# Performance work log

Hardware: AMD Instinct MI355X
Metric: run time of the kernel (lower is better)

Reference implementation:

```python
import jax, jax.numpy as jnp
import numpy as np
import math

B, H, S, D = 1, 8, 2048, 64
LAMBDA_INIT = 0.8 - 0.6 * math.exp(-0.3)  # depth=1
EPS = 1e-5


def _clin(xr, xi, wr, wi, br, bi):
    # complex linear: (wr + i*wi)(xr + i*xi)
    out_r = xr @ wr.T - xi @ wi.T + br
    out_i = xr @ wi.T + xi @ wr.T + bi
    return out_r, out_i


def setup_inputs() -> dict:
    ks = jax.random.split(jax.random.key(0), 24)
    n = lambda i, shp, s=1.0: jax.random.normal(ks[i], shp, jnp.float32) * s
    inv = 1.0 / math.sqrt(D)
    return {
        'q_r': n(0, (B, H, S, D)), 'q_i': n(1, (B, H, S, D)),
        'k_r': n(2, (B, H, S, D)), 'k_i': n(3, (B, H, S, D)),
        'v_r': n(4, (B, H, S, D)), 'v_i': n(5, (B, H, S, D)),
        'pe_q_r': n(6, (B, H, S, D)), 'pe_q_i': n(7, (B, H, S, D)),
        'pe_k_r': n(8, (B, H, S, D)), 'pe_k_i': n(9, (B, H, S, D)),
        'qwr': n(10, (2 * D, D), inv), 'qwi': n(11, (2 * D, D), inv),
        'qbr': jnp.zeros(2 * D), 'qbi': jnp.zeros(2 * D),
        'kwr': n(12, (D, D), inv), 'kwi': n(13, (D, D), inv),
        'kbr': jnp.zeros(D), 'kbi': jnp.zeros(D),
        'vwr': n(14, (D, D), inv), 'vwi': n(15, (D, D), inv),
        'vbr': jnp.zeros(D), 'vbi': jnp.zeros(D),
        'gwr': n(16, (D, D), inv), 'gwi': n(17, (D, D), inv),
        'gbr': jnp.zeros(D), 'gbi': jnp.zeros(D),
        'owr': n(18, (D, D), inv), 'owi': n(19, (D, D), inv),
        'obr': jnp.zeros(D), 'obi': jnp.zeros(D),
        'lq1': n(20, (H,), 0.1), 'lk1': n(21, (H,), 0.1),
        'lq2': n(22, (H,), 0.1), 'lk2': n(23, (H,), 0.1),
        'subw': jnp.ones(2 * D),
    }


def _forward(q_r, q_i, k_r, k_i, v_r, v_i, pe_q_r, pe_q_i, pe_k_r, pe_k_i,
             qwr, qwi, qbr, qbi, kwr, kwi, kbr, kbi, vwr, vwi, vbr, vbi,
             gwr, gwi, gbr, gbi, owr, owi, obr, obi,
             lq1, lk1, lq2, lk2, subw):
    b, h, s, d = q_r.shape
    scale = d ** (-0.5)
    qpr, qpi = _clin(q_r, q_i, qwr, qwi, qbr, qbi)      # [b,h,s,2d]
    kpr, kpi = _clin(k_r, k_i, kwr, kwi, kbr, kbi)      # [b,h,s,d]
    vpr, vpi = _clin(v_r, v_i, vwr, vwi, vbr, vbi)      # [b,h,s,d]
    qpr = qpr + jnp.concatenate([pe_q_r, pe_q_r], -1)
    qpi = qpi + jnp.concatenate([pe_q_i, pe_q_i], -1)
    kpr = kpr + pe_k_r
    kpi = kpi + pe_k_i
    # split two physical heads: view(..., d, 2) interleaves last dim
    qpr = qpr.reshape(b, h, s, d, 2)
    qpi = qpi.reshape(b, h, s, d, 2)
    q1r, q2r = qpr[..., 0], qpr[..., 1]
    q1i, q2i = qpi[..., 0], qpi[..., 1]

    def attn(qr, qi):
        sr = jnp.einsum('bhqd,bhkd->bhqk', qr, kpr) + jnp.einsum('bhqd,bhkd->bhqk', qi, kpi)
        si = jnp.einsum('bhqd,bhkd->bhqk', qi, kpr) - jnp.einsum('bhqd,bhkd->bhqk', qr, kpi)
        scores = jnp.sqrt(sr * sr + si * si + 1e-8) * scale
        return jax.nn.softmax(scores, axis=-1)

    a1 = attn(q1r, q1i)
    a2 = attn(q2r, q2i)
    o1r = a1 @ vpr; o1i = a1 @ vpi
    o2r = a2 @ vpr; o2i = a2 @ vpi
    # NOTE: torch computes a lambda-weighted difference here but immediately
    # overwrites it with the normed slice below, so it never reaches the output.
    cr = jnp.stack([o1r, o2r], -1).reshape(b, h, s, 2 * d)
    ci = jnp.stack([o1i, o2i], -1).reshape(b, h, s, 2 * d)
    rms = jnp.sqrt(jnp.mean(cr * cr + ci * ci, axis=-1, keepdims=True) + EPS)
    nr = cr / rms * subw
    ni = ci / rms * subw
    ar = nr[..., :d]
    ai = ni[..., :d]
    gr, gi = _clin(q_r, q_i, gwr, gwi, gbr, gbi)
    xr = gr * ar - gi * ai
    xi = gr * ai + gi * ar
    out_r, out_i = _clin(xr, xi, owr, owi, obr, obi)
    return out_r, out_i, gr, gi


def reference(q_r, q_i, k_r, k_i, v_r, v_i, pe_q_r, pe_q_i, pe_k_r, pe_k_i,
              qwr, qwi, qbr, qbi, kwr, kwi, kbr, kbi, vwr, vwi, vbr, vbi,
              gwr, gwi, gbr, gbi, owr, owi, obr, obi,
              lq1, lk1, lq2, lk2, subw):
    return _forward(q_r, q_i, k_r, k_i, v_r, v_i, pe_q_r, pe_q_i, pe_k_r, pe_k_i,
                    qwr, qwi, qbr, qbi, kwr, kwi, kbr, kbi, vwr, vwi, vbr, vbi,
                    gwr, gwi, gbr, gbi, owr, owi, obr, obi,
                    lq1, lk1, lq2, lk2, subw)
```

## Files before the change

kernel.cpp:

```cpp
#include <hip/hip_runtime.h>
#include <hip/hip_bf16.h>

#define NH 8
#define SQ 2048
#define HD 64
#define NTOT (NH * SQ * HD)
#define PIT 72

typedef unsigned short u16;
typedef unsigned int u32;
typedef __attribute__((ext_vector_type(8))) unsigned short us8;
typedef __attribute__((ext_vector_type(4))) unsigned short us4v;
typedef __attribute__((ext_vector_type(8))) _Float16 h8;
typedef __attribute__((ext_vector_type(4))) float f4;
typedef __attribute__((ext_vector_type(4))) u32 u4;

#define MFMA_F16 __builtin_amdgcn_mfma_f32_16x16x32_f16

__device__ __forceinline__ u16 f2h(float f) {
    union { _Float16 h; u16 u; } c; c.h = (_Float16)f; return c.u;
}
__device__ __forceinline__ float h2f(u16 u) {
    union { _Float16 h; u16 u; } c; c.u = u; return (float)c.h;
}
__device__ __forceinline__ h8 neg_h8(h8 a) {
    union { h8 h; u4 u; } c; c.h = a;
    c.u ^= 0x80008000u;
    return c.h;
}
__device__ __forceinline__ h8 pack8h(const float* p) {
    float4 a = ((const float4*)p)[0];
    float4 b = ((const float4*)p)[1];
    h8 r;
    r[0] = (_Float16)a.x; r[1] = (_Float16)a.y; r[2] = (_Float16)a.z; r[3] = (_Float16)a.w;
    r[4] = (_Float16)b.x; r[5] = (_Float16)b.y; r[6] = (_Float16)b.z; r[7] = (_Float16)b.w;
    return r;
}

__device__ __forceinline__ int swz8(int row, int chunk) {
    return row * 64 + ((chunk ^ (row & 7)) << 3);
}

struct Afrag { h8 r0, r1, i0, i1, ni0, ni1; };

__global__ __launch_bounds__(256) void proj_kernel(
    const float* __restrict__ q_r, const float* __restrict__ q_i,
    const float* __restrict__ k_r, const float* __restrict__ k_i,
    const float* __restrict__ v_r, const float* __restrict__ v_i,
    const float* __restrict__ pe_q_r, const float* __restrict__ pe_q_i,
    const float* __restrict__ pe_k_r, const float* __restrict__ pe_k_i,
    const float* __restrict__ qwr, const float* __restrict__ qwi,
    const float* __restrict__ qbr, const float* __restrict__ qbi,
    const float* __restrict__ kwr, const float* __restrict__ kwi,
    const float* __restrict__ kbr, const float* __restrict__ kbi,
    const float* __restrict__ vwr, const float* __restrict__ vwi,
    const float* __restrict__ vbr, const float* __restrict__ vbi,
    const float* __restrict__ gwr, const float* __restrict__ gwi,
    const float* __restrict__ gbr, const float* __restrict__ gbi,
    u16* __restrict__ q1r, u16* __restrict__ q1i,
    u16* __restrict__ q2r, u16* __restrict__ q2i,
    u16* __restrict__ kpr, u16* __restrict__ kpi,
    u16* __restrict__ vtr, u16* __restrict__ vti,
    float* __restrict__ out_gr, float* __restrict__ out_gi)
{
    const int t = threadIdx.x;
    const int wv = t >> 6, l = t & 63;
    const int quad = l >> 4, m16 = l & 15;
    const int rowbase = blockIdx.x * 16;
    const int arow = rowbase + m16;
    const int h = rowbase >> 11;
    const int c0 = quad * 8;

    auto loadA = [&](const float* pr, const float* pi) {
        Afrag a;
        const float* rp = pr + arow * 64;
        const float* ip = pi + arow * 64;
        a.r0 = pack8h(rp + c0);      a.r1 = pack8h(rp + 32 + c0);
        a.i0 = pack8h(ip + c0);      a.i1 = pack8h(ip + 32 + c0);
        a.ni0 = neg_h8(a.i0);        a.ni1 = neg_h8(a.i1);
        return a;
    };

    auto ctile = [&](const Afrag& A, const float* wr, const float* wi, int cb,
                     f4& Cr, f4& Ci) {
        const float* wrp = wr + (cb + m16) * 64;
        const float* wip = wi + (cb + m16) * 64;
        h8 Br0 = pack8h(wrp + c0), Br1 = pack8h(wrp + 32 + c0);
        h8 Bi0 = pack8h(wip + c0), Bi1 = pack8h(wip + 32 + c0);
        Cr = (f4)0.f; Ci = (f4)0.f;
        Cr = MFMA_F16(A.r0,  Br0, Cr, 0, 0, 0);
        Cr = MFMA_F16(A.r1,  Br1, Cr, 0, 0, 0);
        Cr = MFMA_F16(A.ni0, Bi0, Cr, 0, 0, 0);
        Cr = MFMA_F16(A.ni1, Bi1, Cr, 0, 0, 0);
        Ci = MFMA_F16(A.r0,  Bi0, Ci, 0, 0, 0);
        Ci = MFMA_F16(A.r1,  Bi1, Ci, 0, 0, 0);
        Ci = MFMA_F16(A.i0,  Br0, Ci, 0, 0, 0);
        Ci = MFMA_F16(A.i1,  Br1, Ci, 0, 0, 0);
    };

    auto qtile = [&](const Afrag& A, int nt) {
        f4 Cr, Ci;
        ctile(A, qwr, qwi, nt * 16, Cr, Ci);
        int c = nt * 16 + m16;
        float br = qbr[c], bi = qbi[c];
        int dd = c >> 1, pc = c & 63;
        u16* dR = (c & 1) ? q2r : q1r;
        u16* dI = (c & 1) ? q2i : q1i;
        #pragma unroll
        for (int r = 0; r < 4; ++r) {
            int g = rowbase + quad * 4 + r;
            dR[g * 64 + dd] = f2h(Cr[r] + br + pe_q_r[g * 64 + pc]);
            dI[g * 64 + dd] = f2h(Ci[r] + bi + pe_q_i[g * 64 + pc]);
        }
    };
    auto ktile = [&](const Afrag& A, int nt) {
        f4 Cr, Ci;
        ctile(A, kwr, kwi, nt * 16, Cr, Ci);
        int c = nt * 16 + m16;
        float br = kbr[c], bi = kbi[c];
        #pragma unroll
        for (int r = 0; r < 4; ++r) {
            int g = rowbase + quad * 4 + r;
            kpr[g * 64 + c] = f2h(Cr[r] + br + pe_k_r[g * 64 + c]);
            kpi[g * 64 + c] = f2h(Ci[r] + bi + pe_k_i[g * 64 + c]);
        }
    };
    auto vtile = [&](const Afrag& A, int nt) {
        f4 Cr, Ci;
        ctile(A, vwr, vwi, nt * 16, Cr, Ci);
        int c = nt * 16 + m16;
        float br = vbr[c], bi = vbi[c];
        int s0 = (rowbase & 2047) + quad * 4;
        size_t tix = (size_t)(h * 64 + c) * 2048 + s0;
        us4v pr, pi;
        #pragma unroll
        for (int r = 0; r < 4; ++r) {
            pr[r] = f2h(Cr[r] + br);
            pi[r] = f2h(Ci[r] + bi);
        }
        *(us4v*)&vtr[tix] = pr;
        *(us4v*)&vti[tix] = pi;
    };
    auto gtile = [&](const Afrag& A, int nt) {
        f4 Cr, Ci;
        ctile(A, gwr, gwi, nt * 16, Cr, Ci);
        int c = nt * 16 + m16;
        float br = gbr[c], bi = gbi[c];
        #pragma unroll
        for (int r = 0; r < 4; ++r) {
            int g = rowbase + quad * 4 + r;
            out_gr[g * 64 + c] = Cr[r] + br;
            out_gi[g * 64 + c] = Ci[r] + bi;
        }
    };

    if (wv == 0) {
        Afrag Aq = loadA(q_r, q_i);
        qtile(Aq, 0); qtile(Aq, 1); qtile(Aq, 2); qtile(Aq, 3); qtile(Aq, 4);
    } else if (wv == 1) {
        Afrag Aq = loadA(q_r, q_i);
        qtile(Aq, 5); qtile(Aq, 6); qtile(Aq, 7);
        gtile(Aq, 0); gtile(Aq, 1);
    } else if (wv == 2) {
        Afrag Ak = loadA(k_r, k_i);
        ktile(Ak, 0); ktile(Ak, 1); ktile(Ak, 2); ktile(Ak, 3);
        Afrag Aq = loadA(q_r, q_i);
        gtile(Aq, 2);
    } else {
        Afrag Av = loadA(v_r, v_i);
        vtile(Av, 0); vtile(Av, 1); vtile(Av, 2); vtile(Av, 3);
        Afrag Aq = loadA(q_r, q_i);
        gtile(Aq, 3);
    }
}

__global__ __launch_bounds__(256) void attn_kernel(
    const u16* __restrict__ q1r, const u16* __restrict__ q1i,
    const u16* __restrict__ q2r, const u16* __restrict__ q2i,
    const u16* __restrict__ kpr, const u16* __restrict__ kpi,
    const u16* __restrict__ vtr, const u16* __restrict__ vti,
    u16* __restrict__ o1r, u16* __restrict__ o1i,
    u16* __restrict__ o2r, u16* __restrict__ o2i)
{
    __shared__ __align__(16) u16 Kr[64 * 64], Ki[64 * 64];
    __shared__ __align__(16) u16 Vr[64 * 64], Vi[64 * 64];
    __shared__ __align__(16) u16 Pb[64 * 64];

    const int t  = threadIdx.x;
    const int qt = blockIdx.x;
    const int br = blockIdx.y;
    const int h  = blockIdx.z;

    const int wq   = t >> 6;
    const int l    = t & 63;
    const int quad = l >> 4;
    const int m    = l & 15;

    const u16* Qsr = br ? q2r : q1r;
    const u16* Qsi = br ? q2i : q1i;
    const int hbase = h * SQ * 64;
    const int qbase = hbase + qt * 64 * 64;
    const int vbase = h * 64 * SQ;

    const u16* qrr = Qsr + qbase + (wq * 16 + m) * 64;
    const u16* qri = Qsi + qbase + (wq * 16 + m) * 64;
    h8 Qr0 = *(const h8*)(qrr + quad * 8);
    h8 Qr1 = *(const h8*)(qrr + 32 + quad * 8);
    h8 Qi0 = *(const h8*)(qri + quad * 8);
    h8 Qi1 = *(const h8*)(qri + 32 + quad * 8);
    h8 nQr0 = neg_h8(Qr0);
    h8 nQr1 = neg_h8(Qr1);

    const int sr0 = t >> 3;
    const int sc  = t & 7;
    us8 rK0, rK1, rC0, rC1, rV0, rV1, rW0, rW1;

    auto issue = [&](int kt) {
        const int kb = hbase + kt * 4096;
        const int vb = vbase + kt * 64;
        const int sc8 = sc * 8;
        rK0 = *(const us8*)(kpr + kb + sr0 * 64 + sc8);
        rK1 = *(const us8*)(kpr + kb + (sr0 + 32) * 64 + sc8);
        rC0 = *(const us8*)(kpi + kb + sr0 * 64 + sc8);
        rC1 = *(const us8*)(kpi + kb + (sr0 + 32) * 64 + sc8);
        rV0 = *(const us8*)(vtr + vb + sr0 * SQ + sc8);
        rV1 = *(const us8*)(vtr + vb + (sr0 + 32) * SQ + sc8);
        rW0 = *(const us8*)(vti + vb + sr0 * SQ + sc8);
        rW1 = *(const us8*)(vti + vb + (sr0 + 32) * SQ + sc8);
    };
    auto commit = [&]() {
        const int o0 = swz8(sr0, sc);
        const int o1 = swz8(sr0 + 32, sc);
        *(us8*)&Kr[o0] = rK0;  *(us8*)&Kr[o1] = rK1;
        *(us8*)&Ki[o0] = rC0;  *(us8*)&Ki[o1] = rC1;
        *(us8*)&Vr[o0] = rV0;  *(us8*)&Vr[o1] = rV1;
        *(us8*)&Vi[o0] = rW0;  *(us8*)&Vi[o1] = rW1;
    };

    float mreg[4], Lp[4];
    #pragma unroll
    for (int r = 0; r < 4; ++r) { mreg[r] = -1e30f; Lp[r] = 0.f; }
    f4 Ovr[4], Ovi[4];
    #pragma unroll
    for (int d = 0; d < 4; ++d) { Ovr[d] = (f4)0.f; Ovi[d] = (f4)0.f; }

    issue(0);

    for (int kt = 0; kt < 32; ++kt) {
        __syncthreads();
        commit();
        if (kt < 31) issue(kt + 1);
        __syncthreads();

        float sv[4][4];
        #pragma unroll
        for (int nt = 0; nt < 4; ++nt) {
            const int kr = nt * 16 + m;
            h8 k0 = *(const h8*)&Kr[swz8(kr, quad)];
            h8 k1 = *(const h8*)&Kr[swz8(kr, quad + 4)];
            h8 c0 = *(const h8*)&Ki[swz8(kr, quad)];
            h8 c1 = *(const h8*)&Ki[swz8(kr, quad + 4)];
            f4 ar = (f4)0.f, ai = (f4)0.f;
            __builtin_amdgcn_s_setprio(1);
            ar = MFMA_F16(Qr0, k0, ar, 0, 0, 0);
            ar = MFMA_F16(Qr1, k1, ar, 0, 0, 0);
            ar = MFMA_F16(Qi0, c0, ar, 0, 0, 0);
            ar = MFMA_F16(Qi1, c1, ar, 0, 0, 0);
            ai = MFMA_F16(Qi0, k0, ai, 0, 0, 0);
            ai = MFMA_F16(Qi1, k1, ai, 0, 0, 0);
            ai = MFMA_F16(nQr0, c0, ai, 0, 0, 0);
            ai = MFMA_F16(nQr1, c1, ai, 0, 0, 0);
            __builtin_amdgcn_s_setprio(0);
            #pragma unroll
            for (int r = 0; r < 4; ++r)
                sv[nt][r] = __builtin_amdgcn_sqrtf(ar[r] * ar[r] + ai[r] * ai[r] + 1e-8f) * 0.125f;
        }

        float rv[4];
        #pragma unroll
        for (int r = 0; r < 4; ++r) {
            float x = fmaxf(fmaxf(sv[0][r], sv[1][r]), fmaxf(sv[2][r], sv[3][r]));
            x = fmaxf(x, __shfl_xor(x, 1));
            x = fmaxf(x, __shfl_xor(x, 2));
            x = fmaxf(x, __shfl_xor(x, 4));
            x = fmaxf(x, __shfl_xor(x, 8));
            rv[r] = x;
        }

        bool need = (rv[0] > mreg[0] + 8.f) | (rv[1] > mreg[1] + 8.f) |
                    (rv[2] > mreg[2] + 8.f) | (rv[3] > mreg[3] + 8.f);
        if (__any(need)) {
            #pragma unroll
            for (int r = 0; r < 4; ++r) {
                float mn = fmaxf(mreg[r], rv[r]);
                float al = __expf(mreg[r] - mn);
                mreg[r] = mn;
                Lp[r] *= al;
                #pragma unroll
                for (int dtr = 0; dtr < 4; ++dtr) { Ovr[dtr][r] *= al; Ovi[dtr][r] *= al; }
            }
        }

        #pragma unroll
        for (int r = 0; r < 4; ++r) {
            const int prow = wq * 16 + quad * 4 + r;
            #pragma unroll
            for (int nt = 0; nt < 4; ++nt) {
                float p = __expf(sv[nt][r] - mreg[r]);
                Lp[r] += p;
                const int col = nt * 16 + m;
                Pb[swz8(prow, col >> 3) + (col & 7)] = f2h(p);
            }
        }

        const int qrow = wq * 16 + m;
        h8 pa0 = *(const h8*)&Pb[swz8(qrow, quad)];
        h8 pa1 = *(const h8*)&Pb[swz8(qrow, quad + 4)];

        #pragma unroll
        for (int dt = 0; dt < 4; ++dt) {
            const int vr_ = dt * 16 + m;
            h8 b0 = *(const h8*)&Vr[swz8(vr_, quad)];
            h8 b1 = *(const h8*)&Vr[swz8(vr_, quad + 4)];
            h8 d0 = *(const h8*)&Vi[swz8(vr_, quad)];
            h8 d1 = *(const h8*)&Vi[swz8(vr_, quad + 4)];
            __builtin_amdgcn_s_setprio(1);
            Ovr[dt] = MFMA_F16(pa0, b0, Ovr[dt], 0, 0, 0);
            Ovr[dt] = MFMA_F16(pa1, b1, Ovr[dt], 0, 0, 0);
            Ovi[dt] = MFMA_F16(pa0, d0, Ovi[dt], 0, 0, 0);
            Ovi[dt] = MFMA_F16(pa1, d1, Ovi[dt], 0, 0, 0);
            __builtin_amdgcn_s_setprio(0);
        }
    }

    {
        #pragma unroll
        for (int r = 0; r < 4; ++r) {
            float x = Lp[r];
            x += __shfl_xor(x, 1);
            x += __shfl_xor(x, 2);
            x += __shfl_xor(x, 4);
            x += __shfl_xor(x, 8);
            Lp[r] = x;
        }
        u16* Dr = br ? o2r : o1r;
        u16* Di = br ? o2i : o1i;
        float inv[4];
        #pragma unroll
        for (int r = 0; r < 4; ++r) inv[r] = 1.f / Lp[r];
        #pragma unroll
        for (int dt = 0; dt < 4; ++dt) {
            #pragma unroll
            for (int r = 0; r < 4; ++r) {
                int q = wq * 16 + quad * 4 + r;
                Dr[qbase + q * 64 + dt * 16 + m] = f2h(Ovr[dt][r] * inv[r]);
                Di[qbase + q * 64 + dt * 16 + m] = f2h(Ovi[dt][r] * inv[r]);
            }
        }
    }
}

__global__ __launch_bounds__(256) void epi_kernel(
    const u16* __restrict__ o1r, const u16* __restrict__ o1i,
    const u16* __restrict__ o2r, const u16* __restrict__ o2i,
    const float* __restrict__ out_gr, const float* __restrict__ out_gi,
    const float* __restrict__ subw,
    const float* __restrict__ owr, const float* __restrict__ owi,
    const float* __restrict__ obr, const float* __restrict__ obi,
    float* __restrict__ out_r, float* __restrict__ out_i)
{
    __shared__ __align__(16) u16 L1r[16][64], L1i[16][64];
    __shared__ __align__(16) u16 L2r[16][64], L2i[16][64];
    __shared__ __align__(16) u16 Xr[16][PIT], Xi[16][PIT];

    const int t = threadIdx.x;
    const int rowbase = blockIdx.x * 16;

    {
        int r = t >> 4, c4 = (t & 15) * 4;
        size_t gi = (size_t)(rowbase + r) * 64 + c4;
        *(us4v*)&L1r[r][c4] = *(const us4v*)(o1r + gi);
        *(us4v*)&L1i[r][c4] = *(const us4v*)(o1i + gi);
        *(us4v*)&L2r[r][c4] = *(const us4v*)(o2r + gi);
        *(us4v*)&L2i[r][c4] = *(const us4v*)(o2i + gi);
    }
    __syncthreads();

    {
        int r = t >> 4, c4 = (t & 15) * 4;
        float ss = 0.f;
        #pragma unroll
        for (int j = 0; j < 4; ++j) {
            float a = h2f(L1r[r][c4 + j]), b = h2f(L1i[r][c4 + j]);
            float c = h2f(L2r[r][c4 + j]), d = h2f(L2i[r][c4 + j]);
            ss += a * a + b * b + c * c + d * d;
        }
        ss += __shfl_xor(ss, 1);
        ss += __shfl_xor(ss, 2);
        ss += __shfl_xor(ss, 4);
        ss += __shfl_xor(ss, 8);
        float inv = 1.f / sqrtf(ss * (1.f / 128.f) + 1e-5f);

        float4 g_r = *(const float4*)(out_gr + (size_t)(rowbase + r) * 64 + c4);
        float4 g_i = *(const float4*)(out_gi + (size_t)(rowbase + r) * 64 + c4);
        const float* grv = (const float*)&g_r;
        const float* giv = (const float*)&g_i;

        us4v xrp, xip;
        #pragma unroll
        for (int j = 0; j < 4; ++j) {
            int c = c4 + j;
            int s = c >> 1;
            float cr_ = (c & 1) ? h2f(L2r[r][s]) : h2f(L1r[r][s]);
            float ci_ = (c & 1) ? h2f(L2i[r][s]) : h2f(L1i[r][s]);
            float sw = subw[c];
            float ar_ = cr_ * inv * sw;
            float ai_ = ci_ * inv * sw;
            xrp[j] = f2h(grv[j] * ar_ - giv[j] * ai_);
            xip[j] = f2h(grv[j] * ai_ + giv[j] * ar_);
        }
        *(us4v*)&Xr[r][c4] = xrp;
        *(us4v*)&Xi[r][c4] = xip;
    }
    __syncthreads();

    const int wv = t >> 6, l = t & 63;
    const int quad = l >> 4, m16 = l & 15;
    const int c0 = quad * 8;

    h8 Ar0 = *(const h8*)&Xr[m16][c0];
    h8 Ar1 = *(const h8*)&Xr[m16][32 + c0];
    h8 Ai0 = *(const h8*)&Xi[m16][c0];
    h8 Ai1 = *(const h8*)&Xi[m16][32 + c0];
    h8 nAi0 = neg_h8(Ai0), nAi1 = neg_h8(Ai1);

    const int c = wv * 16 + m16;
    const float* wrp = owr + c * 64;
    const float* wip = owi + c * 64;
    h8 Br0 = pack8h(wrp + c0), Br1 = pack8h(wrp + 32 + c0);
    h8 Bi0 = pack8h(wip + c0), Bi1 = pack8h(wip + 32 + c0);

    f4 Cr = (f4)0.f, Ci = (f4)0.f;
    Cr = MFMA_F16(Ar0,  Br0, Cr, 0, 0, 0);
    Cr = MFMA_F16(Ar1,  Br1, Cr, 0, 0, 0);
    Cr = MFMA_F16(nAi0, Bi0, Cr, 0, 0, 0);
    Cr = MFMA_F16(nAi1, Bi1, Cr, 0, 0, 0);
    Ci = MFMA_F16(Ar0,  Bi0, Ci, 0, 0, 0);
    Ci = MFMA_F16(Ar1,  Bi1, Ci, 0, 0, 0);
    Ci = MFMA_F16(Ai0,  Br0, Ci, 0, 0, 0);
    Ci = MFMA_F16(Ai1,  Br1, Ci, 0, 0, 0);

    float br_ = obr[c], bi_ = obi[c];
    #pragma unroll
    for (int r = 0; r < 4; ++r) {
        size_t g = (size_t)(rowbase + quad * 4 + r) * 64 + c;
        out_r[g] = Cr[r] + br_;
        out_i[g] = Ci[r] + bi_;
    }
}

extern "C" void kernel_launch(void* const* d_in, const int* in_sizes, int n_in,
                              void* d_out, int out_size, void* d_ws, size_t ws_size,
                              hipStream_t stream)
{
    (void)in_sizes; (void)n_in; (void)out_size; (void)ws_size;

    float* out    = (float*)d_out;
    float* out_r  = out;
    float* out_i  = out + (size_t)NTOT;
    float* out_gr = out + 2 * (size_t)NTOT;
    float* out_gi = out + 3 * (size_t)NTOT;

    char* w = (char*)d_ws;
    const size_t N = (size_t)NTOT;
    u16* q1r = (u16*)w; w += N * 2;
    u16* q1i = (u16*)w; w += N * 2;
    u16* q2r = (u16*)w; w += N * 2;
    u16* q2i = (u16*)w; w += N * 2;
    u16* kpr = (u16*)w; w += N * 2;
    u16* kpi = (u16*)w; w += N * 2;
    u16* vtr = (u16*)w; w += N * 2;
    u16* vti = (u16*)w; w += N * 2;
    u16* o1r = (u16*)w; w += N * 2;
    u16* o1i = (u16*)w; w += N * 2;
    u16* o2r = (u16*)w; w += N * 2;
    u16* o2i = (u16*)w; w += N * 2;

    proj_kernel<<<dim3(1024), dim3(256), 0, stream>>>(
        (const float*)d_in[0], (const float*)d_in[1],
        (const float*)d_in[2], (const float*)d_in[3],
        (const float*)d_in[4], (const float*)d_in[5],
        (const float*)d_in[6], (const float*)d_in[7],
        (const float*)d_in[8], (const float*)d_in[9],
        (const float*)d_in[10], (const float*)d_in[11],
        (const float*)d_in[12], (const float*)d_in[13],
        (const float*)d_in[14], (const float*)d_in[15],
        (const float*)d_in[16], (const float*)d_in[17],
        (const float*)d_in[18], (const float*)d_in[19],
        (const float*)d_in[20], (const float*)d_in[21],
        (const float*)d_in[22], (const float*)d_in[23],
        (const float*)d_in[24], (const float*)d_in[25],
        q1r, q1i, q2r, q2i, kpr, kpi, vtr, vti, out_gr, out_gi);

    attn_kernel<<<dim3(SQ / 64, 2, NH), dim3(256), 0, stream>>>(
        q1r, q1i, q2r, q2i, kpr, kpi, vtr, vti, o1r, o1i, o2r, o2i);

    epi_kernel<<<dim3(1024), dim3(256), 0, stream>>>(
        o1r, o1i, o2r, o2i, out_gr, out_gi,
        (const float*)d_in[34], (const float*)d_in[26], (const float*)d_in[27],
        (const float*)d_in[28], (const float*)d_in[29],
        out_r, out_i);
}
```

Before: 264.1 us.

## Load K/V fragments directly from global memory instead of LDS staging

New measurement: 406.9 us. +54.1%, slower.

```diff
diff --git a/kernel.cpp b/kernel.cpp
--- a/kernel.cpp
+++ b/kernel.cpp
@@ -182,8 +182,6 @@
     u16* __restrict__ o1r, u16* __restrict__ o1i,
     u16* __restrict__ o2r, u16* __restrict__ o2i)
 {
-    __shared__ __align__(16) u16 Kr[64 * 64], Ki[64 * 64];
-    __shared__ __align__(16) u16 Vr[64 * 64], Vi[64 * 64];
     __shared__ __align__(16) u16 Pb[64 * 64];
 
     const int t  = threadIdx.x;
@@ -211,31 +209,10 @@
     h8 nQr0 = neg_h8(Qr0);
     h8 nQr1 = neg_h8(Qr1);
 
-    const int sr0 = t >> 3;
-    const int sc  = t & 7;
-    us8 rK0, rK1, rC0, rC1, rV0, rV1, rW0, rW1;
-
-    auto issue = [&](int kt) {
-        const int kb = hbase + kt * 4096;
-        const int vb = vbase + kt * 64;
-        const int sc8 = sc * 8;
-        rK0 = *(const us8*)(kpr + kb + sr0 * 64 + sc8);
-        rK1 = *(const us8*)(kpr + kb + (sr0 + 32) * 64 + sc8);
-        rC0 = *(const us8*)(kpi + kb + sr0 * 64 + sc8);
-        rC1 = *(const us8*)(kpi + kb + (sr0 + 32) * 64 + sc8);
-        rV0 = *(const us8*)(vtr + vb + sr0 * SQ + sc8);
-        rV1 = *(const us8*)(vtr + vb + (sr0 + 32) * SQ + sc8);
-        rW0 = *(const us8*)(vti + vb + sr0 * SQ + sc8);
-        rW1 = *(const us8*)(vti + vb + (sr0 + 32) * SQ + sc8);
-    };
-    auto commit = [&]() {
-        const int o0 = swz8(sr0, sc);
-        const int o1 = swz8(sr0 + 32, sc);
-        *(us8*)&Kr[o0] = rK0;  *(us8*)&Kr[o1] = rK1;
-        *(us8*)&Ki[o0] = rC0;  *(us8*)&Ki[o1] = rC1;
-        *(us8*)&Vr[o0] = rV0;  *(us8*)&Vr[o1] = rV1;
-        *(us8*)&Vi[o0] = rW0;  *(us8*)&Vi[o1] = rW1;
-    };
+    const u16* bKr = kpr + hbase + m * 64 + quad * 8;
+    const u16* bKi = kpi + hbase + m * 64 + quad * 8;
+    const u16* bVr = vtr + vbase + m * 2048 + quad * 8;
+    const u16* bVi = vti + vbase + m * 2048 + quad * 8;
 
     float mreg[4], Lp[4];
     #pragma unroll
@@ -244,22 +221,14 @@
     #pragma unroll
     for (int d = 0; d < 4; ++d) { Ovr[d] = (f4)0.f; Ovi[d] = (f4)0.f; }
 
-    issue(0);
-
     for (int kt = 0; kt < 32; ++kt) {
-        __syncthreads();
-        commit();
-        if (kt < 31) issue(kt + 1);
-        __syncthreads();
-
         float sv[4][4];
         #pragma unroll
         for (int nt = 0; nt < 4; ++nt) {
-            const int kr = nt * 16 + m;
-            h8 k0 = *(const h8*)&Kr[swz8(kr, quad)];
-            h8 k1 = *(const h8*)&Kr[swz8(kr, quad + 4)];
-            h8 c0 = *(const h8*)&Ki[swz8(kr, quad)];
-            h8 c1 = *(const h8*)&Ki[swz8(kr, quad + 4)];
+            h8 k0 = *(const h8*)(bKr + nt * 1024);
+            h8 k1 = *(const h8*)(bKr + nt * 1024 + 32);
+            h8 c0 = *(const h8*)(bKi + nt * 1024);
+            h8 c1 = *(const h8*)(bKi + nt * 1024 + 32);
             f4 ar = (f4)0.f, ai = (f4)0.f;
             __builtin_amdgcn_s_setprio(1);
             ar = MFMA_F16(Qr0, k0, ar, 0, 0, 0);
@@ -275,6 +244,7 @@
             for (int r = 0; r < 4; ++r)
                 sv[nt][r] = __builtin_amdgcn_sqrtf(ar[r] * ar[r] + ai[r] * ai[r] + 1e-8f) * 0.125f;
         }
+        bKr += 4096; bKi += 4096;
 
         float rv[4];
         #pragma unroll
@@ -319,11 +289,10 @@
 
         #pragma unroll
         for (int dt = 0; dt < 4; ++dt) {
-            const int vr_ = dt * 16 + m;
-            h8 b0 = *(const h8*)&Vr[swz8(vr_, quad)];
-            h8 b1 = *(const h8*)&Vr[swz8(vr_, quad + 4)];
-            h8 d0 = *(const h8*)&Vi[swz8(vr_, quad)];
-            h8 d1 = *(const h8*)&Vi[swz8(vr_, quad + 4)];
+            h8 b0 = *(const h8*)(bVr + dt * 32768);
+            h8 b1 = *(const h8*)(bVr + dt * 32768 + 32);
+            h8 d0 = *(const h8*)(bVi + dt * 32768);
+            h8 d1 = *(const h8*)(bVi + dt * 32768 + 32);
             __builtin_amdgcn_s_setprio(1);
             Ovr[dt] = MFMA_F16(pa0, b0, Ovr[dt], 0, 0, 0);
             Ovr[dt] = MFMA_F16(pa1, b1, Ovr[dt], 0, 0, 0);
@@ -331,6 +300,7 @@
             Ovi[dt] = MFMA_F16(pa1, d1, Ovi[dt], 0, 0, 0);
             __builtin_amdgcn_s_setprio(0);
         }
+        bVr += 64; bVi += 64;
     }
 
     {
```

## Process both head branches per block to share K/V tiles

Applied to the files above, without the earlier changes.

After: 294.1 us. 11.4% more time.

```diff
diff --git a/kernel.cpp b/kernel.cpp
--- a/kernel.cpp
+++ b/kernel.cpp
@@ -174,7 +174,7 @@
     }
 }
 
-__global__ __launch_bounds__(256) void attn_kernel(
+__global__ __launch_bounds__(256, 1) void attn_kernel(
     const u16* __restrict__ q1r, const u16* __restrict__ q1i,
     const u16* __restrict__ q2r, const u16* __restrict__ q2i,
     const u16* __restrict__ kpr, const u16* __restrict__ kpi,
@@ -184,14 +184,15 @@
 {
     __shared__ __align__(16) u16 Kr[64 * 64], Ki[64 * 64];
     __shared__ __align__(16) u16 Vr[64 * 64], Vi[64 * 64];
-    __shared__ __align__(16) u16 Pb[64 * 64];
+    __shared__ __align__(16) u16 Pb[128 * 64];
 
     const int t  = threadIdx.x;
     const int qt = blockIdx.x;
-    const int br = blockIdx.y;
     const int h  = blockIdx.z;
 
     const int wq   = t >> 6;
+    const int br   = wq >> 1;
+    const int rh   = wq & 1;
     const int l    = t & 63;
     const int quad = l >> 4;
     const int m    = l & 15;
@@ -202,14 +203,18 @@
     const int qbase = hbase + qt * 64 * 64;
     const int vbase = h * 64 * SQ;
 
-    const u16* qrr = Qsr + qbase + (wq * 16 + m) * 64;
-    const u16* qri = Qsi + qbase + (wq * 16 + m) * 64;
-    h8 Qr0 = *(const h8*)(qrr + quad * 8);
-    h8 Qr1 = *(const h8*)(qrr + 32 + quad * 8);
-    h8 Qi0 = *(const h8*)(qri + quad * 8);
-    h8 Qi1 = *(const h8*)(qri + 32 + quad * 8);
-    h8 nQr0 = neg_h8(Qr0);
-    h8 nQr1 = neg_h8(Qr1);
+    h8 Qr0[2], Qr1[2], Qi0[2], Qi1[2], nQr0[2], nQr1[2];
+    #pragma unroll
+    for (int rs = 0; rs < 2; ++rs) {
+        const u16* qrr = Qsr + qbase + (rh * 32 + rs * 16 + m) * 64;
+        const u16* qri = Qsi + qbase + (rh * 32 + rs * 16 + m) * 64;
+        Qr0[rs] = *(const h8*)(qrr + quad * 8);
+        Qr1[rs] = *(const h8*)(qrr + 32 + quad * 8);
+        Qi0[rs] = *(const h8*)(qri + quad * 8);
+        Qi1[rs] = *(const h8*)(qri + 32 + quad * 8);
+        nQr0[rs] = neg_h8(Qr0[rs]);
+        nQr1[rs] = neg_h8(Qr1[rs]);
+    }
 
     const int sr0 = t >> 3;
     const int sc  = t & 7;
@@ -237,12 +242,16 @@
         *(us8*)&Vi[o0] = rW0;  *(us8*)&Vi[o1] = rW1;
     };
 
-    float mreg[4], Lp[4];
+    float mreg[2][4], Lp[2][4];
     #pragma unroll
-    for (int r = 0; r < 4; ++r) { mreg[r] = -1e30f; Lp[r] = 0.f; }
-    f4 Ovr[4], Ovi[4];
+    for (int rs = 0; rs < 2; ++rs)
+        #pragma unroll
+        for (int r = 0; r < 4; ++r) { mreg[rs][r] = -1e30f; Lp[rs][r] = 0.f; }
+    f4 Ovr[2][4], Ovi[2][4];
     #pragma unroll
-    for (int d = 0; d < 4; ++d) { Ovr[d] = (f4)0.f; Ovi[d] = (f4)0.f; }
+    for (int rs = 0; rs < 2; ++rs)
+        #pragma unroll
+        for (int d = 0; d < 4; ++d) { Ovr[rs][d] = (f4)0.f; Ovi[rs][d] = (f4)0.f; }
 
     issue(0);
 
@@ -252,7 +261,7 @@
         if (kt < 31) issue(kt + 1);
         __syncthreads();
 
-        float sv[4][4];
+        float sv[2][4][4];
         #pragma unroll
         for (int nt = 0; nt < 4; ++nt) {
             const int kr = nt * 16 + m;
@@ -260,62 +269,78 @@
             h8 k1 = *(const h8*)&Kr[swz8(kr, quad + 4)];
             h8 c0 = *(const h8*)&Ki[swz8(kr, quad)];
             h8 c1 = *(const h8*)&Ki[swz8(kr, quad + 4)];
-            f4 ar = (f4)0.f, ai = (f4)0.f;
             __builtin_amdgcn_s_setprio(1);
-            ar = MFMA_F16(Qr0, k0, ar, 0, 0, 0);
-            ar = MFMA_F16(Qr1, k1, ar, 0, 0, 0);
-            ar = MFMA_F16(Qi0, c0, ar, 0, 0, 0);
-            ar = MFMA_F16(Qi1, c1, ar, 0, 0, 0);
-            ai = MFMA_F16(Qi0, k0, ai, 0, 0, 0);
-            ai = MFMA_F16(Qi1, k1, ai, 0, 0, 0);
-            ai = MFMA_F16(nQr0, c0, ai, 0, 0, 0);
-            ai = MFMA_F16(nQr1, c1, ai, 0, 0, 0);
+            #pragma unroll
+            for (int rs = 0; rs < 2; ++rs) {
+                f4 ar = (f4)0.f, ai = (f4)0.f;
+                ar = MFMA_F16(Qr0[rs], k0, ar, 0, 0, 0);
+                ar = MFMA_F16(Qr1[rs], k1, ar, 0, 0, 0);
+                ar = MFMA_F16(Qi0[rs], c0, ar, 0, 0, 0);
+                ar = MFMA_F16(Qi1[rs], c1, ar, 0, 0, 0);
+                ai = MFMA_F16(Qi0[rs], k0, ai, 0, 0, 0);
+                ai = MFMA_F16(Qi1[rs], k1, ai, 0, 0, 0);
+                ai = MFMA_F16(nQr0[rs], c0, ai, 0, 0, 0);
+                ai = MFMA_F16(nQr1[rs], c1, ai, 0, 0, 0);
+                #pragma unroll
+                for (int r = 0; r < 4; ++r)
+                    sv[rs][nt][r] =
+                        __builtin_amdgcn_sqrtf(ar[r] * ar[r] + ai[r] * ai[r] + 1e-8f) * 0.125f;
+            }
             __builtin_amdgcn_s_setprio(0);
-            #pragma unroll
-            for (int r = 0; r < 4; ++r)
-                sv[nt][r] = __builtin_amdgcn_sqrtf(ar[r] * ar[r] + ai[r] * ai[r] + 1e-8f) * 0.125f;
-        }
-
-        float rv[4];
-        #pragma unroll
-        for (int r = 0; r < 4; ++r) {
-            float x = fmaxf(fmaxf(sv[0][r], sv[1][r]), fmaxf(sv[2][r], sv[3][r]));
-            x = fmaxf(x, __shfl_xor(x, 1));
-            x = fmaxf(x, __shfl_xor(x, 2));
-            x = fmaxf(x, __shfl_xor(x, 4));
-            x = fmaxf(x, __shfl_xor(x, 8));
-            rv[r] = x;
-        }
-
-        bool need = (rv[0] > mreg[0] + 8.f) | (rv[1] > mreg[1] + 8.f) |
-                    (rv[2] > mreg[2] + 8.f) | (rv[3] > mreg[3] + 8.f);
+        }
+
+        float rv[2][4];
+        bool need = false;
+        #pragma unroll
+        for (int rs = 0; rs < 2; ++rs)
+            #pragma unroll
+            for (int r = 0; r < 4; ++r) {
+                float x = fmaxf(fmaxf(sv[rs][0][r], sv[rs][1][r]),
+                                fmaxf(sv[rs][2][r], sv[rs][3][r]));
+                x = fmaxf(x, __shfl_xor(x, 1));
+                x = fmaxf(x, __shfl_xor(x, 2));
+                x = fmaxf(x, __shfl_xor(x, 4));
+                x = fmaxf(x, __shfl_xor(x, 8));
+                rv[rs][r] = x;
+                need |= (x > mreg[rs][r] + 8.f);
+            }
         if (__any(need)) {
             #pragma unroll
+            for (int rs = 0; rs < 2; ++rs)
+                #pragma unroll
+                for (int r = 0; r < 4; ++r) {
+                    float mn = fmaxf(mreg[rs][r], rv[rs][r]);
+                    float al = __expf(mreg[rs][r] - mn);
+                    mreg[rs][r] = mn;
+                    Lp[rs][r] *= al;
+                    #pragma unroll
+                    for (int dt = 0; dt < 4; ++dt) {
+                        Ovr[rs][dt][r] *= al; Ovi[rs][dt][r] *= al;
+                    }
+                }
+        }
+
+        #pragma unroll
+        for (int rs = 0; rs < 2; ++rs)
+            #pragma unroll
             for (int r = 0; r < 4; ++r) {
-                float mn = fmaxf(mreg[r], rv[r]);
-                float al = __expf(mreg[r] - mn);
-                mreg[r] = mn;
-                Lp[r] *= al;
+                const int prow = wq * 32 + rs * 16 + quad * 4 + r;
                 #pragma unroll
-                for (int dtr = 0; dtr < 4; ++dtr) { Ovr[dtr][r] *= al; Ovi[dtr][r] *= al; }
+                for (int nt = 0; nt < 4; ++nt) {
+                    float p = __expf(sv[rs][nt][r] - mreg[rs][r]);
+                    Lp[rs][r] += p;
+                    const int col = nt * 16 + m;
+                    Pb[swz8(prow, col >> 3) + (col & 7)] = f2h(p);
+                }
             }
-        }
-
-        #pragma unroll
-        for (int r = 0; r < 4; ++r) {
-            const int prow = wq * 16 + quad * 4 + r;
-            #pragma unroll
-            for (int nt = 0; nt < 4; ++nt) {
-                float p = __expf(sv[nt][r] - mreg[r]);
-                Lp[r] += p;
-                const int col = nt * 16 + m;
-                Pb[swz8(prow, col >> 3) + (col & 7)] = f2h(p);
-            }
-        }
-
-        const int qrow = wq * 16 + m;
-        h8 pa0 = *(const h8*)&Pb[swz8(qrow, quad)];
-        h8 pa1 = *(const h8*)&Pb[swz8(qrow, quad + 4)];
+
+        h8 pa0[2], pa1[2];
+        #pragma unroll
+        for (int rs = 0; rs < 2; ++rs) {
+            const int qrow = wq * 32 + rs * 16 + m;
+            pa0[rs] = *(const h8*)&Pb[swz8(qrow, quad)];
+            pa1[rs] = *(const h8*)&Pb[swz8(qrow, quad + 4)];
+        }
 
         #pragma unroll
         for (int dt = 0; dt < 4; ++dt) {
@@ -325,36 +350,40 @@
             h8 d0 = *(const h8*)&Vi[swz8(vr_, quad)];
             h8 d1 = *(const h8*)&Vi[swz8(vr_, quad + 4)];
             __builtin_amdgcn_s_setprio(1);
-            Ovr[dt] = MFMA_F16(pa0, b0, Ovr[dt], 0, 0, 0);
-            Ovr[dt] = MFMA_F16(pa1, b1, Ovr[dt], 0, 0, 0);
-            Ovi[dt] = MFMA_F16(pa0, d0, Ovi[dt], 0, 0, 0);
-            Ovi[dt] = MFMA_F16(pa1, d1, Ovi[dt], 0, 0, 0);
+            #pragma unroll
+            for (int rs = 0; rs < 2; ++rs) {
+                Ovr[rs][dt] = MFMA_F16(pa0[rs], b0, Ovr[rs][dt], 0, 0, 0);
+                Ovr[rs][dt] = MFMA_F16(pa1[rs], b1, Ovr[rs][dt], 0, 0, 0);
+                Ovi[rs][dt] = MFMA_F16(pa0[rs], d0, Ovi[rs][dt], 0, 0, 0);
+                Ovi[rs][dt] = MFMA_F16(pa1[rs], d1, Ovi[rs][dt], 0, 0, 0);
+            }
             __builtin_amdgcn_s_setprio(0);
         }
     }
 
     {
-        #pragma unroll
-        for (int r = 0; r < 4; ++r) {
-            float x = Lp[r];
-            x += __shfl_xor(x, 1);
-            x += __shfl_xor(x, 2);
-            x += __shfl_xor(x, 4);
-            x += __shfl_xor(x, 8);
-            Lp[r] = x;
-        }
         u16* Dr = br ? o2r : o1r;
         u16* Di = br ? o2i : o1i;
-        float inv[4];
-        #pragma unroll
-        for (int r = 0; r < 4; ++r) inv[r] = 1.f / Lp[r];
-        #pragma unroll
-        for (int dt = 0; dt < 4; ++dt) {
+        #pragma unroll
+        for (int rs = 0; rs < 2; ++rs) {
+            float inv[4];
             #pragma unroll
             for (int r = 0; r < 4; ++r) {
-                int q = wq * 16 + quad * 4 + r;
-                Dr[qbase + q * 64 + dt * 16 + m] = f2h(Ovr[dt][r] * inv[r]);
-                Di[qbase + q * 64 + dt * 16 + m] = f2h(Ovi[dt][r] * inv[r]);
+                float x = Lp[rs][r];
+                x += __shfl_xor(x, 1);
+                x += __shfl_xor(x, 2);
+                x += __shfl_xor(x, 4);
+                x += __shfl_xor(x, 8);
+                inv[r] = 1.f / x;
+            }
+            #pragma unroll
+            for (int dt = 0; dt < 4; ++dt) {
+                #pragma unroll
+                for (int r = 0; r < 4; ++r) {
+                    int q = rh * 32 + rs * 16 + quad * 4 + r;
+                    Dr[qbase + q * 64 + dt * 16 + m] = f2h(Ovr[rs][dt][r] * inv[r]);
+                    Di[qbase + q * 64 + dt * 16 + m] = f2h(Ovi[rs][dt][r] * inv[r]);
+                }
             }
         }
     }
@@ -502,7 +531,7 @@
         (const float*)d_in[24], (const float*)d_in[25],
         q1r, q1i, q2r, q2i, kpr, kpi, vtr, vti, out_gr, out_gi);
 
-    attn_kernel<<<dim3(SQ / 64, 2, NH), dim3(256), 0, stream>>>(
+    attn_kernel<<<dim3(SQ / 64, 1, NH), dim3(256), 0, stream>>>(
         q1r, q1i, q2r, q2i, kpr, kpi, vtr, vti, o1r, o1i, o2r, o2i);
 
     epi_kernel<<<dim3(1024), dim3(256), 0, stream>>>(
```
